# Performance work log

Measured on AMD Instinct MI355X. Metric: run time of the kernel, lower is better.

The kernel has to match this reference:

```python
import jax, jax.numpy as jnp
import numpy as np

IMG, P, S, E, B = 224, 16, 8, 128, 64
N = (IMG - P) // S + 1          # patches per spatial dim (27)
L = N * N                       # num patches (729)
K = P * P                       # patch area (256)


def _flat_patch_idx():
    # flattened pixel index for each (patch, within-patch) element, shape [L, K]
    base = jnp.arange(N) * S            # top-left corner of each patch row/col
    off = jnp.arange(P)
    rows = base[:, None] + off[None, :]  # [N, P]
    hh = rows[:, None, :, None]          # [N,1,P,1]
    ww = rows[None, :, None, :]          # [1,N,1,P]
    return (hh * IMG + ww).reshape(L, K)  # row-major over patch positions, i*P+j within patch (matches torch Unfold)


def setup_inputs() -> dict:
    key = jax.random.key(0)
    k = jax.random.split(key, 5)
    x = jax.random.normal(k[0], (B, 3, IMG, IMG), dtype=jnp.float32)
    W_enc = jax.random.normal(k[1], (3, E, K), dtype=jnp.float32) * 0.02
    b_enc = jax.random.normal(k[2], (3, E), dtype=jnp.float32) * 0.02
    W_dec = jax.random.normal(k[3], (3, K, E), dtype=jnp.float32) * 0.02
    b_dec = jax.random.normal(k[4], (3, K), dtype=jnp.float32) * 0.02
    return {"x": x, "W_enc": W_enc, "b_enc": b_enc, "W_dec": W_dec, "b_dec": b_dec}


def reference(x, W_enc, b_enc, W_dec, b_dec):
    flat = _flat_patch_idx()                         # [L, K] int indices, static
    Bn = x.shape[0]
    # unfold: gather overlapping patches -> [B, 3, L, K]
    patches = x.reshape(Bn, 3, IMG * IMG)[:, :, flat]
    # per-channel linear encode: [B,3,L,E]
    emb = jnp.einsum('bclk,cek->bcle', patches, W_enc) + b_enc[:, None, :]
    # per-channel linear decode: [B,3,L,K]
    rec = jnp.einsum('bcle,cke->bclk', emb, W_dec) + b_dec[:, None, :]
    # fold: overlap-add scatter back to image
    fi = flat.reshape(-1)
    out = jnp.zeros((Bn, 3, IMG * IMG), x.dtype).at[:, :, fi].add(rec.reshape(Bn, 3, L * K))
    # normalization = fold(unfold(ones)) = per-pixel overlap count
    count = jnp.zeros((IMG * IMG,), x.dtype).at[fi].add(jnp.ones((L * K,), x.dtype))
    return (out / count).reshape(Bn, 3, IMG, IMG)
```

## Files before the change

### kernel.cpp

```cpp
#include <hip/hip_runtime.h>

#define IMG   224
#define IMG2  (IMG*IMG)
#define NN    27
#define KK    256
#define EE    128
#define SCOLS 232
#define RSTR  136

typedef float f32x4 __attribute__((ext_vector_type(4)));
typedef short s16x8 __attribute__((ext_vector_type(8)));
typedef short s16x4 __attribute__((ext_vector_type(4)));

__device__ __forceinline__ unsigned short f2bf(float f) {
    unsigned int u = __float_as_uint(f);
    u = (u + 0x7fffu + ((u >> 16) & 1u)) >> 16;
    return (unsigned short)u;
}
__device__ __forceinline__ float bf2f(unsigned short u) {
    return __uint_as_float((unsigned int)u << 16);
}
__device__ __forceinline__ uint2 pack4(f32x4 r) {
    uint2 u;
    asm("v_cvt_pk_bf16_f32 %0, %1, %2" : "=v"(u.x) : "v"(r.x), "v"(r.y));
    asm("v_cvt_pk_bf16_f32 %0, %1, %2" : "=v"(u.y) : "v"(r.z), "v"(r.w));
    return u;
}

__global__ void pack_M(const float* __restrict__ W_enc, const float* __restrict__ W_dec,
                       const float* __restrict__ b_enc, const float* __restrict__ b_dec,
                       unsigned short* __restrict__ APK, float* __restrict__ v) {
    const int k0 = blockIdx.x*2, c = blockIdx.y, j = threadIdx.x;
    const float* wd0 = W_dec + ((size_t)c*KK + k0)*EE;
    const float* wd1 = wd0 + EE;
    const float* we  = W_enc + (size_t)c*EE*KK + j;
    float a0 = 0.f, a1 = 0.f;
    #pragma unroll 8
    for (int e = 0; e < EE; ++e) {
        float wv = we[(size_t)e*KK];
        a0 = fmaf(wd0[e], wv, a0);
        a1 = fmaf(wd1[e], wv, a1);
    }
    const int jb = j >> 5, g = (j >> 3) & 3, i = j & 7;
    {
        int kf = k0 >> 4, kr = k0 & 15;
        APK[(size_t)c*65536 + (((kf*8 + jb)*64) + g*16 + kr)*8 + i] = f2bf(a0);
        kf = (k0+1) >> 4; kr = (k0+1) & 15;
        APK[(size_t)c*65536 + (((kf*8 + jb)*64) + g*16 + kr)*8 + i] = f2bf(a1);
    }

    __shared__ float pv[256];
    const float* be = b_enc + c*EE;
    pv[j] = (j < EE) ? wd0[j]*be[j] : wd1[j-EE]*be[j-EE];
    __syncthreads();
    for (int off = 64; off > 0; off >>= 1) {
        if ((j & 127) < off) pv[j] += pv[j + off];
        __syncthreads();
    }
    if (j == 0)   v[c*KK + k0]     = pv[0]   + b_dec[c*KK + k0];
    if (j == 128) v[c*KK + k0 + 1] = pv[128] + b_dec[c*KK + k0 + 1];
}

__global__ __launch_bounds__(512, 4)
void patch_ae_loop(const float* __restrict__ x, const unsigned short* __restrict__ APK,
                   const float* __restrict__ v, float* __restrict__ out) {
    const int hid = blockIdx.x;
    const int lid = (hid & 7)*96 + (hid >> 3);
    const int q   = lid & 3;
    const int t2  = lid >> 2;
    const int c   = t2 % 3;
    const int b   = t2 / 3;
    const int s0  = 7*q;

    const int tid  = threadIdx.x;
    const int lane = tid & 63, wave = tid >> 6;

    __shared__ __align__(16) unsigned short ring[32*SCOLS];
    __shared__ __align__(16) unsigned short rec[2][30][RSTR];
    __shared__ __align__(16) float vsh[256];

    if (tid < 256) vsh[tid] = v[c*256 + tid];
    if (tid < RSTR) {
        rec[0][0][tid] = 0; rec[0][28][tid] = 0;
        rec[1][0][tid] = 0; rec[1][28][tid] = 0;
    }

    const int prow   = wave >> 2;
    const int kq     = wave & 3;
    const int kfbase = prow*8 + kq*2;
    const int g = lane >> 4, lr = lane & 15;
    const int jx0 = (g & 1)*8;
    const int c1 = (lr <= 10) ? (128 + 8*lr) : 208;
    const int rowoff = prow ? -8 : 0;

    const int kfu = __builtin_amdgcn_readfirstlane(kfbase);
    const char* abase = (const char*)(APK + (size_t)c*65536) + (size_t)kfu*8192;
    const int v0a = lane*16,       v0b = v0a + 4096;
    const int v1a = v0a + 8192,    v1b = v0a + 12288;

#define ALD(VAR, VOFF, OFFSTR)                                      \
    asm volatile("global_load_dwordx4 %0, %1, %2 offset:" OFFSTR    \
                 : "=v"(VAR) : "v"(VOFF), "s"(abase));

    s16x8 a0_0,a0_1,a0_2,a0_3,a0_4,a0_5,a0_6,a0_7;
    s16x8 a1_0,a1_1,a1_2,a1_3,a1_4,a1_5,a1_6,a1_7;
    ALD(a0_0, v0a, "0")  ALD(a0_1, v0a, "1024") ALD(a0_2, v0a, "2048") ALD(a0_3, v0a, "3072")
    ALD(a0_4, v0b, "0")  ALD(a0_5, v0b, "1024") ALD(a0_6, v0b, "2048") ALD(a0_7, v0b, "3072")
    ALD(a1_0, v1a, "0")  ALD(a1_1, v1a, "1024") ALD(a1_2, v1a, "2048") ALD(a1_3, v1a, "3072")
    ALD(a1_4, v1b, "0")  ALD(a1_5, v1b, "1024") ALD(a1_6, v1b, "2048") ALD(a1_7, v1b, "3072")
#undef ALD

    const float* xb = x + (size_t)(b*3 + c)*IMG2;

    #pragma unroll
    for (int it = 0; it < 2; ++it) {
        int ci = tid + it*512;
        if (ci < 672) {
            int r  = ci / 28, cc = ci - (ci/28)*28;
            int ar = 8*s0 - 8 + r;
            int yr = ar < 0 ? 0 : (ar > 223 ? 223 : ar);
            const float4* src = (const float4*)(xb + (size_t)yr*IMG + cc*8);
            float4 lo = src[0], hi = src[1];
            uint2 u0 = pack4((f32x4){lo.x, lo.y, lo.z, lo.w});
            uint2 u1 = pack4((f32x4){hi.x, hi.y, hi.z, hi.w});
            *((uint4*)&ring[(ar & 31)*SCOLS + cc*8]) = make_uint4(u0.x, u0.y, u1.x, u1.y);
        }
    }
    __syncthreads();
    asm volatile("s_waitcnt vmcnt(0)");
    __builtin_amdgcn_sched_barrier(0);

    const int sr  = tid / 56;
    const int sc4 = tid - 56*(tid/56);

    const int em   = tid % 56, ery = tid / 56;
    const int eq   = em >> 1, ehh = em & 1;
    const int ev1  = (eq < 27), ev0 = (eq > 0);
    const int kl1  = ery*16 + 4*ehh;
    const int kl0  = kl1 + 8;

#define MFMA2(AF, B0, B1, F)                                                             \
        acc[F][0] = __builtin_amdgcn_mfma_f32_16x16x32_bf16(AF, B0, acc[F][0], 0, 0, 0); \
        acc[F][1] = __builtin_amdgcn_mfma_f32_16x16x32_bf16(AF, B1, acc[F][1], 0, 0, 0);

#define MSTEP(JB, A0, A1)                                                            \
        {                                                                            \
            const int jy = 2*(JB) + (g >> 1);                                        \
            const unsigned short* srow = &ring[((rowb + jy) & 31)*SCOLS + jx0];      \
            s16x8 bf0 = *((const s16x8*)&srow[8*lr]);                                \
            s16x8 bf1 = *((const s16x8*)&srow[c1]);                                  \
            __builtin_amdgcn_s_setprio(1);                                           \
            MFMA2(A0, bf0, bf1, 0) MFMA2(A1, bf0, bf1, 1)                            \
            __builtin_amdgcn_s_setprio(0);                                           \
        }

    #pragma unroll 1
    for (int s = s0; s < s0 + 7; ++s) {
        f32x4 ga0;
        if (tid < 448) {
            int yr = 8*(s+2) + sr; if (yr > 223) yr = 223;
            int voffx = yr*(IMG*4) + sc4*16;
            asm volatile("global_load_dwordx4 %0, %1, %2" : "=v"(ga0) : "v"(voffx), "s"(xb));
        }

        f32x4 acc[2][2];
        #pragma unroll
        for (int f = 0; f < 2; ++f)
            #pragma unroll
            for (int pf = 0; pf < 2; ++pf)
                acc[f][pf] = (f32x4){0.f, 0.f, 0.f, 0.f};
        const int rowb = 8*s + rowoff;
        MSTEP(0, a0_0, a1_0)
        MSTEP(1, a0_1, a1_1)
        MSTEP(2, a0_2, a1_2)
        MSTEP(3, a0_3, a1_3)
        MSTEP(4, a0_4, a1_4)
        MSTEP(5, a0_5, a1_5)
        MSTEP(6, a0_6, a1_6)
        MSTEP(7, a0_7, a1_7)

        #pragma unroll
        for (int f = 0; f < 2; ++f) {
            int klocal = kq*32 + f*16 + g*4;
            f32x4 bias = *((const f32x4*)&vsh[prow*128 + klocal]);
            #pragma unroll
            for (int pf = 0; pf < 2; ++pf) {
                f32x4 r = acc[f][pf] + bias;
                int pidx = pf*16 + lr + 1;
                if (pidx >= 28) pidx = 29;
                *((uint2*)&rec[prow][pidx][klocal]) = pack4(r);
            }
        }
        __syncthreads();

        if (tid < 448) {
            const int h0 = (s < 27);
            const int h1 = (s > 0);
            const int shift = (ev0 & ev1) + (h0 & h1);
            const float inv = __int_as_float(0x3f800000 - (shift << 23));
            float sum[4];
            #pragma unroll
            for (int d = 0; d < 4; ++d) sum[d] = 0.f;
            if (h0) {
                s16x4 rrv = *((const s16x4*)&rec[0][eq+1][kl1]);
                s16x4 llv = *((const s16x4*)&rec[0][eq][kl0]);
                #pragma unroll
                for (int d = 0; d < 4; ++d)
                    sum[d] += bf2f((unsigned short)rrv[d]) + bf2f((unsigned short)llv[d]);
            }
            if (h1) {
                s16x4 rrv = *((const s16x4*)&rec[1][eq+1][kl1]);
                s16x4 llv = *((const s16x4*)&rec[1][eq][kl0]);
                #pragma unroll
                for (int d = 0; d < 4; ++d)
                    sum[d] += bf2f((unsigned short)rrv[d]) + bf2f((unsigned short)llv[d]);
            }
            float* orow = out + (size_t)(b*3 + c)*IMG2 + (size_t)(8*s + ery)*IMG + 4*em;
            f32x4 o = {sum[0]*inv, sum[1]*inv, sum[2]*inv, sum[3]*inv};
            *((f32x4*)orow) = o;
        }

        if (tid < 448) {
            asm volatile("s_waitcnt vmcnt(0)");
            __builtin_amdgcn_sched_barrier(0);
            uint2 u0 = pack4(ga0);
            int ar2 = 8*(s+2) + sr;
            *((uint2*)&ring[(ar2 & 31)*SCOLS + sc4*4]) = u0;
        }
        __syncthreads();
    }
#undef MSTEP
#undef MFMA2
}

extern "C" void kernel_launch(void* const* d_in, const int* in_sizes, int n_in,
                              void* d_out, int out_size, void* d_ws, size_t ws_size,
                              hipStream_t stream) {
    (void)in_sizes; (void)n_in; (void)out_size; (void)ws_size;
    const float* x     = (const float*)d_in[0];
    const float* W_enc = (const float*)d_in[1];
    const float* b_enc = (const float*)d_in[2];
    const float* W_dec = (const float*)d_in[3];
    const float* b_dec = (const float*)d_in[4];
    float* out = (float*)d_out;

    float*          v   = (float*)d_ws;
    unsigned short* APK = (unsigned short*)((char*)d_ws + 4096);

    pack_M<<<dim3(KK/2, 3), 256, 0, stream>>>(W_enc, W_dec, b_enc, b_dec, APK, v);
    patch_ae_loop<<<dim3(768), 512, 0, stream>>>(x, APK, v, out);
}
```

Baseline: 40.42 us.

## Double-buffer reconstruction tile and defer epilogue to remove a barrier per step

```diff
diff --git a/kernel.cpp b/kernel.cpp
--- a/kernel.cpp
+++ b/kernel.cpp
@@ -76,13 +76,15 @@
     const int lane = tid & 63, wave = tid >> 6;
 
     __shared__ __align__(16) unsigned short ring[32*SCOLS];
-    __shared__ __align__(16) unsigned short rec[2][30][RSTR];
+    __shared__ __align__(16) unsigned short rec[2][2][30][RSTR];
     __shared__ __align__(16) float vsh[256];
 
     if (tid < 256) vsh[tid] = v[c*256 + tid];
     if (tid < RSTR) {
-        rec[0][0][tid] = 0; rec[0][28][tid] = 0;
-        rec[1][0][tid] = 0; rec[1][28][tid] = 0;
+        rec[0][0][0][tid] = 0; rec[0][0][28][tid] = 0;
+        rec[0][1][0][tid] = 0; rec[0][1][28][tid] = 0;
+        rec[1][0][0][tid] = 0; rec[1][0][28][tid] = 0;
+        rec[1][1][0][tid] = 0; rec[1][1][28][tid] = 0;
     }
 
     const int prow   = wave >> 2;
@@ -138,6 +140,35 @@
     const int ev1  = (eq < 27), ev0 = (eq > 0);
     const int kl1  = ery*16 + 4*ehh;
     const int kl0  = kl1 + 8;
+
+#define EPILOGUE(ES)                                                                     \
+        if (tid < 448) {                                                                 \
+            const int par = (ES) & 1;                                                    \
+            const int h0 = ((ES) < 27);                                                  \
+            const int h1 = ((ES) > 0);                                                   \
+            const int shift = (ev0 & ev1) + (h0 & h1);                                   \
+            const float inv = __int_as_float(0x3f800000 - (shift << 23));                \
+            float sum[4];                                                                \
+            _Pragma("unroll")                                                            \
+            for (int d = 0; d < 4; ++d) sum[d] = 0.f;                                    \
+            if (h0) {                                                                    \
+                s16x4 rrv = *((const s16x4*)&rec[par][0][eq+1][kl1]);                    \
+                s16x4 llv = *((const s16x4*)&rec[par][0][eq][kl0]);                      \
+                _Pragma("unroll")                                                        \
+                for (int d = 0; d < 4; ++d)                                              \
+                    sum[d] += bf2f((unsigned short)rrv[d]) + bf2f((unsigned short)llv[d]); \
+            }                                                                            \
+            if (h1) {                                                                    \
+                s16x4 rrv = *((const s16x4*)&rec[par][1][eq+1][kl1]);                    \
+                s16x4 llv = *((const s16x4*)&rec[par][1][eq][kl0]);                      \
+                _Pragma("unroll")                                                        \
+                for (int d = 0; d < 4; ++d)                                              \
+                    sum[d] += bf2f((unsigned short)rrv[d]) + bf2f((unsigned short)llv[d]); \
+            }                                                                            \
+            float* orow = out + (size_t)(b*3 + c)*IMG2 + (size_t)(8*(ES) + ery)*IMG + 4*em; \
+            f32x4 o = {sum[0]*inv, sum[1]*inv, sum[2]*inv, sum[3]*inv};                  \
+            *((f32x4*)orow) = o;                                                         \
+        }
 
 #define MFMA2(AF, B0, B1, F)                                                             \
         acc[F][0] = __builtin_amdgcn_mfma_f32_16x16x32_bf16(AF, B0, acc[F][0], 0, 0, 0); \
@@ -179,46 +210,23 @@
         MSTEP(6, a0_6, a1_6)
         MSTEP(7, a0_7, a1_7)
 
-        #pragma unroll
-        for (int f = 0; f < 2; ++f) {
-            int klocal = kq*32 + f*16 + g*4;
-            f32x4 bias = *((const f32x4*)&vsh[prow*128 + klocal]);
+        {
+            const int par = s & 1;
             #pragma unroll
-            for (int pf = 0; pf < 2; ++pf) {
-                f32x4 r = acc[f][pf] + bias;
-                int pidx = pf*16 + lr + 1;
-                if (pidx >= 28) pidx = 29;
-                *((uint2*)&rec[prow][pidx][klocal]) = pack4(r);
+            for (int f = 0; f < 2; ++f) {
+                int klocal = kq*32 + f*16 + g*4;
+                f32x4 bias = *((const f32x4*)&vsh[prow*128 + klocal]);
+                #pragma unroll
+                for (int pf = 0; pf < 2; ++pf) {
+                    f32x4 r = acc[f][pf] + bias;
+                    int pidx = pf*16 + lr + 1;
+                    if (pidx >= 28) pidx = 29;
+                    *((uint2*)&rec[par][prow][pidx][klocal]) = pack4(r);
+                }
             }
         }
-        __syncthreads();
-
-        if (tid < 448) {
-            const int h0 = (s < 27);
-            const int h1 = (s > 0);
-            const int shift = (ev0 & ev1) + (h0 & h1);
-            const float inv = __int_as_float(0x3f800000 - (shift << 23));
-            float sum[4];
-            #pragma unroll
-            for (int d = 0; d < 4; ++d) sum[d] = 0.f;
-            if (h0) {
-                s16x4 rrv = *((const s16x4*)&rec[0][eq+1][kl1]);
-                s16x4 llv = *((const s16x4*)&rec[0][eq][kl0]);
-                #pragma unroll
-                for (int d = 0; d < 4; ++d)
-                    sum[d] += bf2f((unsigned short)rrv[d]) + bf2f((unsigned short)llv[d]);
-            }
-            if (h1) {
-                s16x4 rrv = *((const s16x4*)&rec[1][eq+1][kl1]);
-                s16x4 llv = *((const s16x4*)&rec[1][eq][kl0]);
-                #pragma unroll
-                for (int d = 0; d < 4; ++d)
-                    sum[d] += bf2f((unsigned short)rrv[d]) + bf2f((unsigned short)llv[d]);
-            }
-            float* orow = out + (size_t)(b*3 + c)*IMG2 + (size_t)(8*s + ery)*IMG + 4*em;
-            f32x4 o = {sum[0]*inv, sum[1]*inv, sum[2]*inv, sum[3]*inv};
-            *((f32x4*)orow) = o;
-        }
+
+        if (s > s0) { EPILOGUE(s-1) }
 
         if (tid < 448) {
             asm volatile("s_waitcnt vmcnt(0)");
@@ -227,10 +235,14 @@
             int ar2 = 8*(s+2) + sr;
             *((uint2*)&ring[(ar2 & 31)*SCOLS + sc4*4]) = u0;
         }
+
         __syncthreads();
     }
+
+    EPILOGUE(s0 + 6)
 #undef MSTEP
 #undef MFMA2
+#undef EPILOGUE
 }
 
 extern "C" void kernel_launch(void* const* d_in, const int* in_sizes, int n_in,
```

After: 40.32 us (median of 3 runs). About the same (-0.2%).
